# Kernel optimization log

Measured on AMD Instinct MI355X. Metric: run time of the kernel, lower is better.

Reference implementation:

```python
import jax, jax.numpy as jnp
import numpy as np

EMBED_DIM = 192
NUM_HEADS = 6
HEAD_DIM = EMBED_DIM // NUM_HEADS
WIN = (7, 7, 7)
N = WIN[0] * WIN[1] * WIN[2]  # 343
B = 512
NW = 64  # windows per volume (mask leading dim); B % NW == 0
SCALE = HEAD_DIM ** (-0.5)


def _relative_position_index():
    coords = np.stack(np.meshgrid(np.arange(WIN[0]), np.arange(WIN[1]), np.arange(WIN[2]), indexing='ij'))
    flat = coords.reshape(3, -1)
    rel = flat[:, :, None] - flat[:, None, :]            # (3, N, N)
    rel = np.transpose(rel, (1, 2, 0)).astype(np.int64)  # (N, N, 3)
    rel[:, :, 0] += WIN[0] - 1
    rel[:, :, 1] += WIN[1] - 1
    rel[:, :, 2] += WIN[2] - 1
    rel[:, :, 0] *= (2 * WIN[1] - 1) * (2 * WIN[2] - 1)
    rel[:, :, 1] *= 2 * WIN[2] - 1
    return rel.sum(-1)  # (N, N) ints in [0, (2Wh-1)(2Ww-1)(2Wd-1))


def setup_inputs() -> dict:
    key = jax.random.key(0)
    ks = jax.random.split(key, 7)
    table_size = (2 * WIN[0] - 1) * (2 * WIN[1] - 1) * (2 * WIN[2] - 1)  # 2197
    return {
        'x': jax.random.normal(ks[0], (B, N, EMBED_DIM), dtype=jnp.float32),
        'mask': jax.random.normal(ks[1], (NW, N, N), dtype=jnp.float32),
        'qkv_w': jax.random.normal(ks[2], (EMBED_DIM, 3 * EMBED_DIM), dtype=jnp.float32) * 0.02,
        'qkv_b': jnp.zeros((3 * EMBED_DIM,), dtype=jnp.float32),
        'proj_w': jax.random.normal(ks[3], (EMBED_DIM, EMBED_DIM), dtype=jnp.float32) * 0.02,
        'proj_b': jnp.zeros((EMBED_DIM,), dtype=jnp.float32),
        'bias_table': jax.random.normal(ks[4], (table_size, NUM_HEADS), dtype=jnp.float32) * 0.02,
        'rpi': jnp.asarray(_relative_position_index(), dtype=jnp.int32),  # (N, N)
    }


def reference(x, mask, qkv_w, qkv_b, proj_w, proj_b, bias_table, rpi):
    Bn, Nn, C = x.shape
    # QKV projection
    qkv = x @ qkv_w + qkv_b                                   # (B, N, 3C)
    qkv = qkv.reshape(Bn, Nn, 3, NUM_HEADS, HEAD_DIM)
    qkv = jnp.transpose(qkv, (2, 0, 3, 1, 4))                 # (3, B, H, N, hd)
    q, k, v = qkv[0], qkv[1], qkv[2]
    attn = jnp.einsum('bhnd,bhmd->bhnm', q * SCALE, k)        # (B, H, N, N)
    # gather relative position bias: (N*N, H) -> (1, H, N, N)
    rel_bias = bias_table[rpi.reshape(-1)].reshape(Nn, Nn, NUM_HEADS)
    attn = attn + jnp.transpose(rel_bias, (2, 0, 1))[None]
    # per-window mask addition
    nw = mask.shape[0]
    attn = attn.reshape(Bn // nw, nw, NUM_HEADS, Nn, Nn)
    attn = attn + mask[None, :, None, :, :]
    attn = attn.reshape(Bn, NUM_HEADS, Nn, Nn)
    attn = jax.nn.softmax(attn, axis=-1)
    out = jnp.einsum('bhnm,bhmd->bnhd', attn, v).reshape(Bn, Nn, C)
    return out @ proj_w + proj_b
```

## Files before the change

### kernel.cpp

```cpp
#include <hip/hip_runtime.h>
#include <stdint.h>

#define N_TOK 343
#define NPAD  352
#define EMB   192
#define HD    32
#define SCALE 0.17677669529663689f

typedef __attribute__((ext_vector_type(8))) short short8;
typedef __attribute__((ext_vector_type(4))) short short4v;
typedef __attribute__((ext_vector_type(4))) float floatx4;

__device__ __forceinline__ short f2bf(float f) {
  union { float f; unsigned u; } v; v.f = f;
  unsigned r = v.u + 0x7fffu + ((v.u >> 16) & 1u);
  return (short)(r >> 16);
}
__device__ __forceinline__ float bf2f(short s) {
  union { unsigned u; float f; } v;
  v.u = ((unsigned)(unsigned short)s) << 16;
  return v.f;
}
__device__ __forceinline__ unsigned pack2(float a, float b) {
  return (unsigned)(unsigned short)f2bf(a) | ((unsigned)(unsigned short)f2bf(b) << 16);
}

__global__ void prep_weights(const float* __restrict__ qkv_w,
                             const float* __restrict__ qkv_b,
                             const float* __restrict__ proj_w,
                             short* __restrict__ wpack,
                             float* __restrict__ bpack,
                             short* __restrict__ WpT)
{
  int i0 = blockIdx.x * blockDim.x + threadIdx.x;
  int stride = gridDim.x * blockDim.x;
  for (int idx = i0; idx < 110592; idx += stride) {
    int k = idx % 192;
    int t = idx / 192;
    int n = t % 32;
    int mat = (t / 32) % 3;
    int h = t / 96;
    float v = qkv_w[k * 576 + mat * 192 + h * 32 + n];
    if (mat == 0) v *= SCALE;
    wpack[idx] = f2bf(v);
  }
  for (int idx = i0; idx < 36864; idx += stride) {
    int k = idx % 192;
    int n = idx / 192;
    WpT[idx] = f2bf(proj_w[k * 192 + n]);
  }
  for (int idx = i0; idx < 576; idx += stride) {
    int d = idx % 32;
    int mat = (idx / 32) % 3;
    int h = idx / 96;
    float v = qkv_b[mat * 192 + h * 32 + d];
    if (mat == 0) v *= SCALE;
    bpack[idx] = v;
  }
}

__global__ void prep_bias(const float* __restrict__ bias_table,
                          const int* __restrict__ rpi,
                          short* __restrict__ biasH)
{
  int p = blockIdx.x * blockDim.x + threadIdx.x;
  int h = blockIdx.y;
  if (p < N_TOK * N_TOK) {
    int t = rpi[p];
    biasH[h * (N_TOK * N_TOK) + p] = f2bf(bias_table[t * 6 + h]);
  }
}

__global__ __launch_bounds__(256, 2) void fused_attn(
    const float* __restrict__ x,
    const float* __restrict__ mask,
    const short* __restrict__ wpack,
    const float* __restrict__ bpack,
    const short* __restrict__ biasH,
    short* __restrict__ AO)
{
  const int tid  = threadIdx.x;
  const int wave = tid >> 6;
  const int lane = tid & 63;
  const int l16  = lane & 15;
  const int quad = lane >> 4;

  int id   = blockIdx.x;
  int xcd  = id & 7;
  int j    = id >> 3;
  int w_id = xcd * 8 + (j / 48);
  int r    = j % 48;
  int h    = r % 6;
  int b    = (r / 6) * 64 + w_id;

  extern __shared__ short smem_s[];
  short* Kl = smem_s;
  short* Vt = smem_s + 14080;
  short* Wv = smem_s + 25600 + wave * 2048;
  short* Qs = Wv;
  short* Pb = Wv + 640;

  const float* bsrc = bpack + h * 96;
  const float bq0 = bsrc[l16],      bq1 = bsrc[16 + l16];
  const float bk0 = bsrc[32 + l16], bk1 = bsrc[48 + l16];
  const float bv0 = bsrc[64 + l16], bv1 = bsrc[80 + l16];

  const float* xb = x + (size_t)b * (N_TOK * EMB);
  const short* wh = wpack + h * 18432;
  unsigned qreg[6][4];

#pragma unroll 1
  for (int ch = 0; ch < 6; ++ch) {
    int r0 = ch * 64 + wave * 16;
    if (r0 >= NPAD) continue;
    int row = r0 + l16;
    bool rok = row < N_TOK;
    const float* xr = xb + (size_t)row * EMB;

    short8 af[6];
#pragma unroll
    for (int kk = 0; kk < 6; ++kk) {
      const float* xp = xr + kk * 32 + quad * 8;
      float4 a0 = rok ? *(const float4*)xp       : make_float4(0.f, 0.f, 0.f, 0.f);
      float4 a1 = rok ? *(const float4*)(xp + 4) : make_float4(0.f, 0.f, 0.f, 0.f);
      short8 t;
      t[0] = f2bf(a0.x); t[1] = f2bf(a0.y); t[2] = f2bf(a0.z); t[3] = f2bf(a0.w);
      t[4] = f2bf(a1.x); t[5] = f2bf(a1.y); t[6] = f2bf(a1.z); t[7] = f2bf(a1.w);
      af[kk] = t;
    }

    int mg = r0 + quad * 4;
#pragma unroll
    for (int mat = 0; mat < 3; ++mat) {
      const short* wb = wh + mat * 6144;
      floatx4 acc0 = {0.f, 0.f, 0.f, 0.f}, acc1 = {0.f, 0.f, 0.f, 0.f};
#pragma unroll
      for (int kk = 0; kk < 6; ++kk) {
        short8 b0 = *(const short8*)(wb + l16 * 192 + kk * 32 + quad * 8);
        short8 b1 = *(const short8*)(wb + (16 + l16) * 192 + kk * 32 + quad * 8);
        acc0 = __builtin_amdgcn_mfma_f32_16x16x32_bf16(af[kk], b0, acc0, 0, 0, 0);
        acc1 = __builtin_amdgcn_mfma_f32_16x16x32_bf16(af[kk], b1, acc1, 0, 0, 0);
      }
      if (mat == 0) {
#pragma unroll
        for (int reg = 0; reg < 4; ++reg)
          qreg[ch][reg] = pack2(acc0[reg] + bq0, acc1[reg] + bq1);
      } else if (mat == 1) {
#pragma unroll
        for (int reg = 0; reg < 4; ++reg) {
          int m = mg + reg;
          bool mv = m < N_TOK;
          Kl[m * 40 + l16]      = f2bf(mv ? acc0[reg] + bk0 : 0.f);
          Kl[m * 40 + 16 + l16] = f2bf(mv ? acc1[reg] + bk1 : 0.f);
        }
      } else {
        short4v sv0, sv1;
#pragma unroll
        for (int reg = 0; reg < 4; ++reg) {
          int m = mg + reg;
          bool mv = m < N_TOK;
          sv0[reg] = f2bf(mv ? acc0[reg] + bv0 : 0.f);
          sv1[reg] = f2bf(mv ? acc1[reg] + bv1 : 0.f);
        }
        *(short4v*)(Vt + l16 * 360 + mg)        = sv0;
        *(short4v*)(Vt + (16 + l16) * 360 + mg) = sv1;
      }
    }
  }
  __syncthreads();

  const float* mbase = mask + (size_t)(b & 63) * (N_TOK * N_TOK);
  const short* bbase = biasH + (size_t)h * (N_TOK * N_TOK);

#pragma unroll 1
  for (int c = wave; c < 22; c += 4) {
    const int m0 = c * 16;
    const int jx = c >> 2;

#pragma unroll
    for (int reg = 0; reg < 4; ++reg) {
      unsigned p = qreg[jx][reg];
      int rr = quad * 4 + reg;
      Qs[rr * 40 + l16]      = (short)(p & 0xffffu);
      Qs[rr * 40 + 16 + l16] = (short)(p >> 16);
    }
    short8 qf = *(const short8*)(Qs + l16 * 40 + quad * 8);

    const float* mr[4];
    const short* br[4];
#pragma unroll
    for (int reg = 0; reg < 4; ++reg) {
      int m = m0 + quad * 4 + reg;
      int mc = (m < N_TOK) ? m : (N_TOK - 1);
      mr[reg] = mbase + mc * N_TOK;
      br[reg] = bbase + mc * N_TOK;
    }

    float rsum4[4] = {0.f, 0.f, 0.f, 0.f};
    floatx4 o0 = {0.f, 0.f, 0.f, 0.f}, o1 = {0.f, 0.f, 0.f, 0.f};

    float nm0[4], nm1[4], nb0[4], nb1[4];
#pragma unroll
    for (int reg = 0; reg < 4; ++reg) {
      nm0[reg] = mr[reg][l16];
      nm1[reg] = mr[reg][16 + l16];
      nb0[reg] = bf2f(br[reg][l16]);
      nb1[reg] = bf2f(br[reg][16 + l16]);
    }

#pragma unroll 2
    for (int g = 0; g < 11; ++g) {
      float xm0[4], xm1[4], xb0[4], xb1[4];
#pragma unroll
      for (int reg = 0; reg < 4; ++reg) {
        xm0[reg] = nm0[reg]; xm1[reg] = nm1[reg];
        xb0[reg] = nb0[reg]; xb1[reg] = nb1[reg];
      }
      if (g < 10) {
        int c0 = (g + 1) * 32 + l16;
        int c1t = (g + 1) * 32 + 16 + l16;
        int c1 = (c1t < N_TOK) ? c1t : (N_TOK - 1);
#pragma unroll
        for (int reg = 0; reg < 4; ++reg) {
          nm0[reg] = mr[reg][c0];
          nm1[reg] = mr[reg][c1];
          nb0[reg] = bf2f(br[reg][c0]);
          nb1[reg] = bf2f(br[reg][c1]);
        }
      }

      const int k0 = g * 32;
      short8 kf0 = *(const short8*)(Kl + (k0 + l16) * 40 + quad * 8);
      short8 kf1 = *(const short8*)(Kl + (k0 + 16 + l16) * 40 + quad * 8);
      floatx4 zz = {0.f, 0.f, 0.f, 0.f};
      floatx4 s0 = __builtin_amdgcn_mfma_f32_16x16x32_bf16(qf, kf0, zz, 0, 0, 0);
      floatx4 s1 = __builtin_amdgcn_mfma_f32_16x16x32_bf16(qf, kf1, zz, 0, 0, 0);

      bool p1ok = (k0 + 16 + l16) < N_TOK;
      short* pb = Pb + (g & 1) * 640;
#pragma unroll
      for (int reg = 0; reg < 4; ++reg) {
        float e0 = exp2f((s0[reg] + xm0[reg] + xb0[reg]) * 1.44269504f);
        float e1 = p1ok ? exp2f((s1[reg] + xm1[reg] + xb1[reg]) * 1.44269504f) : 0.f;
        rsum4[reg] += e0 + e1;
        int rr = quad * 4 + reg;
        pb[rr * 40 + l16]      = f2bf(e0);
        pb[rr * 40 + 16 + l16] = f2bf(e1);
      }
      short8 pf  = *(const short8*)(pb + l16 * 40 + quad * 8);
      short8 vf0 = *(const short8*)(Vt + l16 * 360 + k0 + quad * 8);
      short8 vf1 = *(const short8*)(Vt + (16 + l16) * 360 + k0 + quad * 8);
      o0 = __builtin_amdgcn_mfma_f32_16x16x32_bf16(pf, vf0, o0, 0, 0, 0);
      o1 = __builtin_amdgcn_mfma_f32_16x16x32_bf16(pf, vf1, o1, 0, 0, 0);
    }

#pragma unroll
    for (int reg = 0; reg < 4; ++reg) {
      float s = rsum4[reg];
#pragma unroll
      for (int off = 1; off < 16; off <<= 1)
        s += __shfl_xor(s, off, 16);
      rsum4[reg] = 1.0f / s;
    }

#pragma unroll
    for (int reg = 0; reg < 4; ++reg) {
      int m = m0 + quad * 4 + reg;
      if (m < N_TOK) {
        short* dst = AO + ((size_t)b * N_TOK + m) * EMB + h * HD;
        dst[l16]      = f2bf(o0[reg] * rsum4[reg]);
        dst[16 + l16] = f2bf(o1[reg] * rsum4[reg]);
      }
    }
  }
}

__global__ __launch_bounds__(256) void proj_gemm(
    const short* __restrict__ AO,
    const short* __restrict__ WpT,
    const float* __restrict__ proj_b,
    float* __restrict__ out)
{
  __shared__ short As[64 * 200];
  const int tid  = threadIdx.x;
  const int wave = tid >> 6;
  const int lane = tid & 63;
  const int l16  = lane & 15;
  const int quad = lane >> 4;
  const int mb = blockIdx.x;

  const short* Ab = AO + (size_t)mb * (64 * EMB);
  for (int i = tid * 8; i < 64 * EMB; i += 2048) {
    uint4 va = *(const uint4*)(Ab + i);
    int rr = i / EMB, cc = i - rr * EMB;
    *(uint4*)(As + rr * 200 + cc) = va;
  }
  __syncthreads();

  short8 af[6];
#pragma unroll
  for (int kk = 0; kk < 6; ++kk)
    af[kk] = *(const short8*)(As + (wave * 16 + l16) * 200 + kk * 32 + quad * 8);

#pragma unroll 1
  for (int nt = 0; nt < 12; ++nt) {
    floatx4 acc = {0.f, 0.f, 0.f, 0.f};
#pragma unroll
    for (int kk = 0; kk < 6; ++kk) {
      short8 bf = *(const short8*)(WpT + (nt * 16 + l16) * EMB + kk * 32 + quad * 8);
      acc = __builtin_amdgcn_mfma_f32_16x16x32_bf16(af[kk], bf, acc, 0, 0, 0);
    }
    int colg = nt * 16 + l16;
    float pb = proj_b[colg];
    int mrow = mb * 64 + wave * 16 + quad * 4;
#pragma unroll
    for (int reg = 0; reg < 4; ++reg) {
      out[(size_t)(mrow + reg) * EMB + colg] = acc[reg] + pb;
    }
  }
}

extern "C" void kernel_launch(void* const* d_in, const int* in_sizes, int n_in,
                              void* d_out, int out_size, void* d_ws, size_t ws_size,
                              hipStream_t stream) {
  (void)in_sizes; (void)n_in; (void)out_size; (void)ws_size;
  const float* x        = (const float*)d_in[0];
  const float* mask     = (const float*)d_in[1];
  const float* qkv_w    = (const float*)d_in[2];
  const float* qkv_b    = (const float*)d_in[3];
  const float* proj_w   = (const float*)d_in[4];
  const float* proj_b   = (const float*)d_in[5];
  const float* bias_tab = (const float*)d_in[6];
  const int*   rpi      = (const int*)d_in[7];

  char* ws = (char*)d_ws;
  short* wpack = (short*)(ws);
  float* bpack = (float*)(ws + 221184);
  short* WpT   = (short*)(ws + 223488);
  short* biasH = (short*)(ws + 297216);
  short* AO    = (short*)(ws + 1709056);

  hipLaunchKernelGGL(prep_weights, dim3(128), dim3(256), 0, stream,
                     qkv_w, qkv_b, proj_w, wpack, bpack, WpT);
  hipLaunchKernelGGL(prep_bias, dim3(460, 6), dim3(256), 0, stream,
                     bias_tab, rpi, biasH);

  const int lds_bytes = 67584;
  (void)hipFuncSetAttribute((const void*)fused_attn,
                            hipFuncAttributeMaxDynamicSharedMemorySize, lds_bytes);
  hipLaunchKernelGGL(fused_attn, dim3(3072), dim3(256), lds_bytes, stream,
                     x, mask, wpack, bpack, biasH, AO);

  hipLaunchKernelGGL(proj_gemm, dim3(2744), dim3(256), 0, stream,
                     AO, WpT, proj_b, (float*)d_out);
}
```

Baseline: 900.7 us.

## Transpose attention MFMA layout, pad mask/bias rows, fold log2e, drop LDS staging

Measured after the change: 920.3 us. 1.02x slower.

```diff
diff --git a/kernel.cpp b/kernel.cpp
--- a/kernel.cpp
+++ b/kernel.cpp
@@ -6,9 +6,11 @@
 #define EMB   192
 #define HD    32
 #define SCALE 0.17677669529663689f
+#define L2E   1.44269504088896341f
 
 typedef __attribute__((ext_vector_type(8))) short short8;
 typedef __attribute__((ext_vector_type(4))) short short4v;
+typedef __attribute__((ext_vector_type(2))) unsigned uint2v;
 typedef __attribute__((ext_vector_type(4))) float floatx4;
 
 __device__ __forceinline__ short f2bf(float f) {
@@ -21,8 +23,29 @@
   v.u = ((unsigned)(unsigned short)s) << 16;
   return v.f;
 }
-__device__ __forceinline__ unsigned pack2(float a, float b) {
-  return (unsigned)(unsigned short)f2bf(a) | ((unsigned)(unsigned short)f2bf(b) << 16);
+__device__ __forceinline__ unsigned cvtpk(float lo, float hi) {
+  unsigned r;
+  asm("v_cvt_pk_bf16_f32 %0, %1, %2" : "=v"(r) : "v"(lo), "v"(hi));
+  return r;
+}
+union U8 { unsigned u[4]; short8 s; };
+__device__ __forceinline__ short8 mk8(unsigned a, unsigned b, unsigned c, unsigned d) {
+  U8 t; t.u[0] = a; t.u[1] = b; t.u[2] = c; t.u[3] = d; return t.s;
+}
+
+__device__ __forceinline__ void quad_transpose(unsigned& w0, unsigned& w1,
+                                               unsigned& w2, unsigned& w3,
+                                               int quad) {
+  unsigned s0 = (quad & 2) ? w0 : w2;
+  unsigned s1 = (quad & 2) ? w1 : w3;
+  s0 = (unsigned)__shfl_xor((int)s0, 32);
+  s1 = (unsigned)__shfl_xor((int)s1, 32);
+  if (quad & 2) { w0 = s0; w1 = s1; } else { w2 = s0; w3 = s1; }
+  unsigned t0 = (quad & 1) ? w0 : w2;
+  unsigned t1 = (quad & 1) ? w1 : w3;
+  t0 = (unsigned)__shfl_xor((int)t0, 16);
+  t1 = (unsigned)__shfl_xor((int)t1, 16);
+  if (quad & 1) { w0 = t0; w1 = t1; } else { w2 = t0; w3 = t1; }
 }
 
 __global__ void prep_weights(const float* __restrict__ qkv_w,
@@ -41,7 +64,7 @@
     int mat = (t / 32) % 3;
     int h = t / 96;
     float v = qkv_w[k * 576 + mat * 192 + h * 32 + n];
-    if (mat == 0) v *= SCALE;
+    if (mat == 0) v *= SCALE * L2E;
     wpack[idx] = f2bf(v);
   }
   for (int idx = i0; idx < 36864; idx += stride) {
@@ -54,29 +77,44 @@
     int mat = (idx / 32) % 3;
     int h = idx / 96;
     float v = qkv_b[mat * 192 + h * 32 + d];
-    if (mat == 0) v *= SCALE;
+    if (mat == 0) v *= SCALE * L2E;
     bpack[idx] = v;
   }
 }
 
 __global__ void prep_bias(const float* __restrict__ bias_table,
                           const int* __restrict__ rpi,
-                          short* __restrict__ biasH)
+                          short* __restrict__ biasP)
 {
   int p = blockIdx.x * blockDim.x + threadIdx.x;
   int h = blockIdx.y;
-  if (p < N_TOK * N_TOK) {
-    int t = rpi[p];
-    biasH[h * (N_TOK * N_TOK) + p] = f2bf(bias_table[t * 6 + h]);
-  }
-}
-
-__global__ __launch_bounds__(256, 2) void fused_attn(
+  if (p < N_TOK * NPAD) {
+    int q = p / NPAD, k = p - q * NPAD;
+    short v = 0;
+    if (k < N_TOK) v = f2bf(bias_table[(size_t)rpi[q * N_TOK + k] * 6 + h] * L2E);
+    biasP[(size_t)h * (N_TOK * NPAD) + p] = v;
+  }
+}
+
+__global__ void prep_mask(const float* __restrict__ mask,
+                          float* __restrict__ maskP)
+{
+  int i0 = blockIdx.x * blockDim.x + threadIdx.x;
+  int stride = gridDim.x * blockDim.x;
+  const int total = 64 * N_TOK * NPAD;
+  for (int idx = i0; idx < total; idx += stride) {
+    int k = idx % NPAD;
+    int t = idx / NPAD;
+    maskP[idx] = (k < N_TOK) ? mask[(size_t)t * N_TOK + k] * L2E : -1e30f;
+  }
+}
+
+__global__ __launch_bounds__(256, 3) void fused_attn(
     const float* __restrict__ x,
-    const float* __restrict__ mask,
+    const float* __restrict__ maskP,
     const short* __restrict__ wpack,
     const float* __restrict__ bpack,
-    const short* __restrict__ biasH,
+    const short* __restrict__ biasP,
     short* __restrict__ AO)
 {
   const int tid  = threadIdx.x;
@@ -96,20 +134,23 @@
   extern __shared__ short smem_s[];
   short* Kl = smem_s;
   short* Vt = smem_s + 14080;
-  short* Wv = smem_s + 25600 + wave * 2048;
-  short* Qs = Wv;
-  short* Pb = Wv + 640;
 
   const float* bsrc = bpack + h * 96;
-  const float bq0 = bsrc[l16],      bq1 = bsrc[16 + l16];
-  const float bk0 = bsrc[32 + l16], bk1 = bsrc[48 + l16];
+  float bqA[4], bqB[4], bkA[4], bkB[4];
+#pragma unroll
+  for (int rg = 0; rg < 4; ++rg) {
+    bqA[rg] = bsrc[quad * 4 + rg];
+    bqB[rg] = bsrc[16 + quad * 4 + rg];
+    bkA[rg] = bsrc[32 + quad * 4 + rg];
+    bkB[rg] = bsrc[48 + quad * 4 + rg];
+  }
   const float bv0 = bsrc[64 + l16], bv1 = bsrc[80 + l16];
 
   const float* xb = x + (size_t)b * (N_TOK * EMB);
   const short* wh = wpack + h * 18432;
   unsigned qreg[6][4];
 
-#pragma unroll 1
+#pragma unroll
   for (int ch = 0; ch < 6; ++ch) {
     int r0 = ch * 64 + wave * 16;
     if (r0 >= NPAD) continue;
@@ -121,19 +162,49 @@
 #pragma unroll
     for (int kk = 0; kk < 6; ++kk) {
       const float* xp = xr + kk * 32 + quad * 8;
-      float4 a0 = rok ? *(const float4*)xp       : make_float4(0.f, 0.f, 0.f, 0.f);
-      float4 a1 = rok ? *(const float4*)(xp + 4) : make_float4(0.f, 0.f, 0.f, 0.f);
-      short8 t;
-      t[0] = f2bf(a0.x); t[1] = f2bf(a0.y); t[2] = f2bf(a0.z); t[3] = f2bf(a0.w);
-      t[4] = f2bf(a1.x); t[5] = f2bf(a1.y); t[6] = f2bf(a1.z); t[7] = f2bf(a1.w);
-      af[kk] = t;
-    }
-
-    int mg = r0 + quad * 4;
-#pragma unroll
-    for (int mat = 0; mat < 3; ++mat) {
-      const short* wb = wh + mat * 6144;
-      floatx4 acc0 = {0.f, 0.f, 0.f, 0.f}, acc1 = {0.f, 0.f, 0.f, 0.f};
+      floatx4 a0 = rok ? *(const floatx4*)xp       : (floatx4){0.f, 0.f, 0.f, 0.f};
+      floatx4 a1 = rok ? *(const floatx4*)(xp + 4) : (floatx4){0.f, 0.f, 0.f, 0.f};
+      af[kk] = mk8(cvtpk(a0[0], a0[1]), cvtpk(a0[2], a0[3]),
+                   cvtpk(a1[0], a1[1]), cvtpk(a1[2], a1[3]));
+    }
+
+    {
+      const short* wb = wh;
+      floatx4 acc0 = {0.f,0.f,0.f,0.f}, acc1 = {0.f,0.f,0.f,0.f};
+#pragma unroll
+      for (int kk = 0; kk < 6; ++kk) {
+        short8 b0 = *(const short8*)(wb + l16 * 192 + kk * 32 + quad * 8);
+        short8 b1 = *(const short8*)(wb + (16 + l16) * 192 + kk * 32 + quad * 8);
+        acc0 = __builtin_amdgcn_mfma_f32_16x16x32_bf16(b0, af[kk], acc0, 0, 0, 0);
+        acc1 = __builtin_amdgcn_mfma_f32_16x16x32_bf16(b1, af[kk], acc1, 0, 0, 0);
+      }
+      qreg[ch][0] = cvtpk(acc0[0] + bqA[0], acc0[1] + bqA[1]);
+      qreg[ch][1] = cvtpk(acc0[2] + bqA[2], acc0[3] + bqA[3]);
+      qreg[ch][2] = cvtpk(acc1[0] + bqB[0], acc1[1] + bqB[1]);
+      qreg[ch][3] = cvtpk(acc1[2] + bqB[2], acc1[3] + bqB[3]);
+    }
+    {
+      const short* wb = wh + 6144;
+      floatx4 acc0 = {0.f,0.f,0.f,0.f}, acc1 = {0.f,0.f,0.f,0.f};
+#pragma unroll
+      for (int kk = 0; kk < 6; ++kk) {
+        short8 b0 = *(const short8*)(wb + l16 * 192 + kk * 32 + quad * 8);
+        short8 b1 = *(const short8*)(wb + (16 + l16) * 192 + kk * 32 + quad * 8);
+        acc0 = __builtin_amdgcn_mfma_f32_16x16x32_bf16(b0, af[kk], acc0, 0, 0, 0);
+        acc1 = __builtin_amdgcn_mfma_f32_16x16x32_bf16(b1, af[kk], acc1, 0, 0, 0);
+      }
+      unsigned c0 = cvtpk(acc0[0] + bkA[0], acc0[1] + bkA[1]);
+      unsigned c1 = cvtpk(acc0[2] + bkA[2], acc0[3] + bkA[3]);
+      unsigned c2 = cvtpk(acc1[0] + bkB[0], acc1[1] + bkB[1]);
+      unsigned c3 = cvtpk(acc1[2] + bkB[2], acc1[3] + bkB[3]);
+      if (!rok) { c0 = 0u; c1 = 0u; c2 = 0u; c3 = 0u; }
+      uint2v p0 = {c0, c1}, p1 = {c2, c3};
+      *(uint2v*)(Kl + row * 40 + quad * 4)      = p0;
+      *(uint2v*)(Kl + row * 40 + 16 + quad * 4) = p1;
+    }
+    {
+      const short* wb = wh + 12288;
+      floatx4 acc0 = {0.f,0.f,0.f,0.f}, acc1 = {0.f,0.f,0.f,0.f};
 #pragma unroll
       for (int kk = 0; kk < 6; ++kk) {
         short8 b0 = *(const short8*)(wb + l16 * 192 + kk * 32 + quad * 8);
@@ -141,136 +212,98 @@
         acc0 = __builtin_amdgcn_mfma_f32_16x16x32_bf16(af[kk], b0, acc0, 0, 0, 0);
         acc1 = __builtin_amdgcn_mfma_f32_16x16x32_bf16(af[kk], b1, acc1, 0, 0, 0);
       }
-      if (mat == 0) {
-#pragma unroll
-        for (int reg = 0; reg < 4; ++reg)
-          qreg[ch][reg] = pack2(acc0[reg] + bq0, acc1[reg] + bq1);
-      } else if (mat == 1) {
-#pragma unroll
-        for (int reg = 0; reg < 4; ++reg) {
-          int m = mg + reg;
-          bool mv = m < N_TOK;
-          Kl[m * 40 + l16]      = f2bf(mv ? acc0[reg] + bk0 : 0.f);
-          Kl[m * 40 + 16 + l16] = f2bf(mv ? acc1[reg] + bk1 : 0.f);
-        }
-      } else {
-        short4v sv0, sv1;
-#pragma unroll
-        for (int reg = 0; reg < 4; ++reg) {
-          int m = mg + reg;
-          bool mv = m < N_TOK;
-          sv0[reg] = f2bf(mv ? acc0[reg] + bv0 : 0.f);
-          sv1[reg] = f2bf(mv ? acc1[reg] + bv1 : 0.f);
-        }
-        *(short4v*)(Vt + l16 * 360 + mg)        = sv0;
-        *(short4v*)(Vt + (16 + l16) * 360 + mg) = sv1;
-      }
+      int mg = r0 + quad * 4;
+      float t0 = (mg + 0 < N_TOK) ? acc0[0] + bv0 : 0.f;
+      float t1 = (mg + 1 < N_TOK) ? acc0[1] + bv0 : 0.f;
+      float t2 = (mg + 2 < N_TOK) ? acc0[2] + bv0 : 0.f;
+      float t3 = (mg + 3 < N_TOK) ? acc0[3] + bv0 : 0.f;
+      float u0 = (mg + 0 < N_TOK) ? acc1[0] + bv1 : 0.f;
+      float u1 = (mg + 1 < N_TOK) ? acc1[1] + bv1 : 0.f;
+      float u2 = (mg + 2 < N_TOK) ? acc1[2] + bv1 : 0.f;
+      float u3 = (mg + 3 < N_TOK) ? acc1[3] + bv1 : 0.f;
+      uint2v sv0 = {cvtpk(t0, t1), cvtpk(t2, t3)};
+      uint2v sv1 = {cvtpk(u0, u1), cvtpk(u2, u3)};
+      *(uint2v*)(Vt + l16 * 360 + mg)        = sv0;
+      *(uint2v*)(Vt + (16 + l16) * 360 + mg) = sv1;
     }
   }
   __syncthreads();
 
-  const float* mbase = mask + (size_t)(b & 63) * (N_TOK * N_TOK);
-  const short* bbase = biasH + (size_t)h * (N_TOK * N_TOK);
-
-#pragma unroll 1
-  for (int c = wave; c < 22; c += 4) {
+  const float* mwin = maskP + (size_t)(b & 63) * (N_TOK * NPAD);
+  const short* bhed = biasP + (size_t)h * (N_TOK * NPAD);
+
+#pragma unroll
+  for (int jx = 0; jx < 6; ++jx) {
+    int c = jx * 4 + wave;
+    if (c >= 22) continue;
     const int m0 = c * 16;
-    const int jx = c >> 2;
-
-#pragma unroll
-    for (int reg = 0; reg < 4; ++reg) {
-      unsigned p = qreg[jx][reg];
-      int rr = quad * 4 + reg;
-      Qs[rr * 40 + l16]      = (short)(p & 0xffffu);
-      Qs[rr * 40 + 16 + l16] = (short)(p >> 16);
-    }
-    short8 qf = *(const short8*)(Qs + l16 * 40 + quad * 8);
-
-    const float* mr[4];
-    const short* br[4];
-#pragma unroll
-    for (int reg = 0; reg < 4; ++reg) {
-      int m = m0 + quad * 4 + reg;
-      int mc = (m < N_TOK) ? m : (N_TOK - 1);
-      mr[reg] = mbase + mc * N_TOK;
-      br[reg] = bbase + mc * N_TOK;
-    }
-
-    float rsum4[4] = {0.f, 0.f, 0.f, 0.f};
-    floatx4 o0 = {0.f, 0.f, 0.f, 0.f}, o1 = {0.f, 0.f, 0.f, 0.f};
-
-    float nm0[4], nm1[4], nb0[4], nb1[4];
-#pragma unroll
-    for (int reg = 0; reg < 4; ++reg) {
-      nm0[reg] = mr[reg][l16];
-      nm1[reg] = mr[reg][16 + l16];
-      nb0[reg] = bf2f(br[reg][l16]);
-      nb1[reg] = bf2f(br[reg][16 + l16]);
-    }
+
+    unsigned qw0 = qreg[jx][0], qw1 = qreg[jx][1], qw2 = qreg[jx][2], qw3 = qreg[jx][3];
+    quad_transpose(qw0, qw1, qw2, qw3, quad);
+    short8 qf = mk8(qw0, qw1, qw2, qw3);
+
+    const int q  = m0 + l16;
+    const int qc = (q < N_TOK) ? q : (N_TOK - 1);
+    const float* mrow = mwin + (size_t)qc * NPAD;
+    const short* brow = bhed + (size_t)qc * NPAD;
+
+    float rsum = 0.f;
+    floatx4 o0 = {0.f,0.f,0.f,0.f}, o1 = {0.f,0.f,0.f,0.f};
+
+    floatx4 nm0 = *(const floatx4*)(mrow + quad * 4);
+    floatx4 nm1 = *(const floatx4*)(mrow + 16 + quad * 4);
+    short4v nb0 = *(const short4v*)(brow + quad * 4);
+    short4v nb1 = *(const short4v*)(brow + 16 + quad * 4);
 
 #pragma unroll 2
     for (int g = 0; g < 11; ++g) {
-      float xm0[4], xm1[4], xb0[4], xb1[4];
-#pragma unroll
-      for (int reg = 0; reg < 4; ++reg) {
-        xm0[reg] = nm0[reg]; xm1[reg] = nm1[reg];
-        xb0[reg] = nb0[reg]; xb1[reg] = nb1[reg];
-      }
+      const int k0 = g * 32;
+      floatx4 xm0 = nm0, xm1 = nm1;
+      short4v xb0 = nb0, xb1 = nb1;
       if (g < 10) {
-        int c0 = (g + 1) * 32 + l16;
-        int c1t = (g + 1) * 32 + 16 + l16;
-        int c1 = (c1t < N_TOK) ? c1t : (N_TOK - 1);
-#pragma unroll
-        for (int reg = 0; reg < 4; ++reg) {
-          nm0[reg] = mr[reg][c0];
-          nm1[reg] = mr[reg][c1];
-          nb0[reg] = bf2f(br[reg][c0]);
-          nb1[reg] = bf2f(br[reg][c1]);
-        }
-      }
-
-      const int k0 = g * 32;
+        nm0 = *(const floatx4*)(mrow + k0 + 32 + quad * 4);
+        nm1 = *(const floatx4*)(mrow + k0 + 48 + quad * 4);
+        nb0 = *(const short4v*)(brow + k0 + 32 + quad * 4);
+        nb1 = *(const short4v*)(brow + k0 + 48 + quad * 4);
+      }
+
       short8 kf0 = *(const short8*)(Kl + (k0 + l16) * 40 + quad * 8);
       short8 kf1 = *(const short8*)(Kl + (k0 + 16 + l16) * 40 + quad * 8);
-      floatx4 zz = {0.f, 0.f, 0.f, 0.f};
-      floatx4 s0 = __builtin_amdgcn_mfma_f32_16x16x32_bf16(qf, kf0, zz, 0, 0, 0);
-      floatx4 s1 = __builtin_amdgcn_mfma_f32_16x16x32_bf16(qf, kf1, zz, 0, 0, 0);
-
-      bool p1ok = (k0 + 16 + l16) < N_TOK;
-      short* pb = Pb + (g & 1) * 640;
-#pragma unroll
-      for (int reg = 0; reg < 4; ++reg) {
-        float e0 = exp2f((s0[reg] + xm0[reg] + xb0[reg]) * 1.44269504f);
-        float e1 = p1ok ? exp2f((s1[reg] + xm1[reg] + xb1[reg]) * 1.44269504f) : 0.f;
-        rsum4[reg] += e0 + e1;
-        int rr = quad * 4 + reg;
-        pb[rr * 40 + l16]      = f2bf(e0);
-        pb[rr * 40 + 16 + l16] = f2bf(e1);
-      }
-      short8 pf  = *(const short8*)(pb + l16 * 40 + quad * 8);
       short8 vf0 = *(const short8*)(Vt + l16 * 360 + k0 + quad * 8);
       short8 vf1 = *(const short8*)(Vt + (16 + l16) * 360 + k0 + quad * 8);
-      o0 = __builtin_amdgcn_mfma_f32_16x16x32_bf16(pf, vf0, o0, 0, 0, 0);
-      o1 = __builtin_amdgcn_mfma_f32_16x16x32_bf16(pf, vf1, o1, 0, 0, 0);
-    }
-
-#pragma unroll
-    for (int reg = 0; reg < 4; ++reg) {
-      float s = rsum4[reg];
-#pragma unroll
-      for (int off = 1; off < 16; off <<= 1)
-        s += __shfl_xor(s, off, 16);
-      rsum4[reg] = 1.0f / s;
-    }
-
-#pragma unroll
-    for (int reg = 0; reg < 4; ++reg) {
-      int m = m0 + quad * 4 + reg;
-      if (m < N_TOK) {
-        short* dst = AO + ((size_t)b * N_TOK + m) * EMB + h * HD;
-        dst[l16]      = f2bf(o0[reg] * rsum4[reg]);
-        dst[16 + l16] = f2bf(o1[reg] * rsum4[reg]);
-      }
+
+      floatx4 zz = {0.f,0.f,0.f,0.f};
+      floatx4 s0 = __builtin_amdgcn_mfma_f32_16x16x32_bf16(kf0, qf, zz, 0, 0, 0);
+      floatx4 s1 = __builtin_amdgcn_mfma_f32_16x16x32_bf16(kf1, qf, zz, 0, 0, 0);
+
+      float e0r[4], e1r[4];
+#pragma unroll
+      for (int rg = 0; rg < 4; ++rg) {
+        e0r[rg] = __builtin_amdgcn_exp2f(s0[rg] + (xm0[rg] + bf2f(xb0[rg])));
+        e1r[rg] = __builtin_amdgcn_exp2f(s1[rg] + (xm1[rg] + bf2f(xb1[rg])));
+        rsum += e0r[rg] + e1r[rg];
+      }
+      unsigned w0 = cvtpk(e0r[0], e0r[1]);
+      unsigned w1 = cvtpk(e0r[2], e0r[3]);
+      unsigned w2 = cvtpk(e1r[0], e1r[1]);
+      unsigned w3 = cvtpk(e1r[2], e1r[3]);
+      quad_transpose(w0, w1, w2, w3, quad);
+      short8 pf = mk8(w0, w1, w2, w3);
+
+      o0 = __builtin_amdgcn_mfma_f32_16x16x32_bf16(vf0, pf, o0, 0, 0, 0);
+      o1 = __builtin_amdgcn_mfma_f32_16x16x32_bf16(vf1, pf, o1, 0, 0, 0);
+    }
+
+    rsum += __shfl_xor(rsum, 16);
+    rsum += __shfl_xor(rsum, 32);
+    float rinv = 1.0f / rsum;
+
+    if (q < N_TOK) {
+      short* dst = AO + ((size_t)b * N_TOK + q) * EMB + h * HD;
+      uint2v d0 = {cvtpk(o0[0] * rinv, o0[1] * rinv), cvtpk(o0[2] * rinv, o0[3] * rinv)};
+      uint2v d1 = {cvtpk(o1[0] * rinv, o1[1] * rinv), cvtpk(o1[2] * rinv, o1[3] * rinv)};
+      *(uint2v*)(dst + quad * 4)      = d0;
+      *(uint2v*)(dst + 16 + quad * 4) = d1;
     }
   }
 }
@@ -337,19 +370,22 @@
   short* wpack = (short*)(ws);
   float* bpack = (float*)(ws + 221184);
   short* WpT   = (short*)(ws + 223488);
-  short* biasH = (short*)(ws + 297216);
-  short* AO    = (short*)(ws + 1709056);
+  short* biasP = (short*)(ws + 297216);
+  float* maskP = (float*)(ws + 1746048);
+  short* AO    = (short*)(ws + 32654464);
 
   hipLaunchKernelGGL(prep_weights, dim3(128), dim3(256), 0, stream,
                      qkv_w, qkv_b, proj_w, wpack, bpack, WpT);
-  hipLaunchKernelGGL(prep_bias, dim3(460, 6), dim3(256), 0, stream,
-                     bias_tab, rpi, biasH);
-
-  const int lds_bytes = 67584;
+  hipLaunchKernelGGL(prep_bias, dim3(472, 6), dim3(256), 0, stream,
+                     bias_tab, rpi, biasP);
+  hipLaunchKernelGGL(prep_mask, dim3(2048), dim3(256), 0, stream,
+                     mask, maskP);
+
+  const int lds_bytes = 51200;
   (void)hipFuncSetAttribute((const void*)fused_attn,
                             hipFuncAttributeMaxDynamicSharedMemorySize, lds_bytes);
   hipLaunchKernelGGL(fused_attn, dim3(3072), dim3(256), lds_bytes, stream,
-                     x, mask, wpack, bpack, biasH, AO);
+                     x, maskP, wpack, bpack, biasP, AO);
 
   hipLaunchKernelGGL(proj_gemm, dim3(2744), dim3(256), 0, stream,
                      AO, WpT, proj_b, (float*)d_out);
```
